# Kernel tuning notes

Measured on AMD Instinct MI355X. Metric: run time of the kernel, lower is better.

The kernel has to match this reference:

```python
import jax, jax.numpy as jnp
import numpy as np

B, S, D = 2, 2048, 1024
H, DQK, DV = 16, 64, 64
DECAY = 0.85


def _fractal_weights(seq_len: int, decay: float) -> np.ndarray:
    # Dragon-curve hierarchical weights: earlier (coarser) positions get higher
    # weight; weight decays by `decay` per hierarchy level. Normalized to sum 1,
    # matching DragonCurveGenerator.get_hierarchical_weights semantics.
    idx = np.arange(seq_len)
    level = np.floor(np.log2(idx + 1)).astype(np.int32)
    w = decay ** level.astype(np.float32)
    return (w / w.sum()).astype(np.float32)


def setup_inputs() -> dict:
    key = jax.random.key(0)
    kx, kq, kk, kv, ko = jax.random.split(key, 5)
    s = 1.0 / np.sqrt(D)
    return {
        "x": jax.random.normal(kx, (B, S, D), dtype=jnp.float32),
        "Wq": jax.random.normal(kq, (D, H * DQK), dtype=jnp.float32) * s,
        "Wk": jax.random.normal(kk, (D, H * DQK), dtype=jnp.float32) * s,
        "Wv": jax.random.normal(kv, (D, H * DV), dtype=jnp.float32) * s,
        "Wo": jax.random.normal(ko, (H * DV, D), dtype=jnp.float32) * s,
        "fractal_weights": jnp.asarray(_fractal_weights(S, DECAY)),
    }


def reference(x, Wq, Wk, Wv, Wo, fractal_weights):
    b, s, _ = x.shape
    # Projections (Linear with bias=False); weights stored as (in, out).
    Q = (x @ Wq).reshape(b, s, H, DQK).transpose(0, 2, 1, 3)  # [B,H,S,Dqk]
    K = (x @ Wk).reshape(b, s, H, DQK).transpose(0, 2, 1, 3)
    V = (x @ Wv).reshape(b, s, H, DV).transpose(0, 2, 1, 3)   # [B,H,S,Dv]
    scale = 1.0 / jnp.sqrt(jnp.asarray(DQK, dtype=x.dtype))
    scores = jnp.einsum("bhqd,bhkd->bhqk", Q, K) * scale      # [B,H,S,S]
    # Multiplicative per-key fractal bias applied BEFORE softmax.
    scores = scores * fractal_weights[None, None, None, :]
    attn = jax.nn.softmax(scores, axis=-1)
    out = jnp.einsum("bhqk,bhkd->bhqd", attn, V)               # [B,H,S,Dv]
    out = out.transpose(0, 2, 1, 3).reshape(b, s, H * DV)
    return out @ Wo                                            # [B,S,D]
```

## Files before the change

kernel.cpp:

```cpp
#include <hip/hip_runtime.h>
#include <hip/hip_bf16.h>
#include <stdint.h>

#define B_  2
#define S_  2048
#define D_  1024
#define H_  16
#define DH_ 64

typedef __attribute__((ext_vector_type(8))) __bf16    bf16x8;
typedef __attribute__((ext_vector_type(8))) _Float16  f16x8;
typedef __attribute__((ext_vector_type(4))) _Float16  f16x4;
typedef __attribute__((ext_vector_type(2))) __fp16    fp16x2;
typedef __attribute__((ext_vector_type(4))) float     f32x4;

__device__ inline unsigned short f2bf(float f) {
    union { float f; uint32_t u; } v; v.f = f;
    uint32_t r = (v.u + 0x7fffu + ((v.u >> 16) & 1u)) >> 16;
    return (unsigned short)r;
}

__device__ __forceinline__ void g2l16(const unsigned short* g, unsigned short* l) {
    __builtin_amdgcn_global_load_lds(
        (const __attribute__((address_space(1))) unsigned int*)g,
        (__attribute__((address_space(3))) unsigned int*)l,
        16, 0, 0);
}


__global__ void convert_x(const float* __restrict__ x, unsigned short* __restrict__ xb, int n) {
    int i = (blockIdx.x * blockDim.x + threadIdx.x) * 4;
    if (i < n) {
        float4 v = *(const float4*)(x + i);
        ushort4 o;
        o.x = f2bf(v.x); o.y = f2bf(v.y); o.z = f2bf(v.z); o.w = f2bf(v.w);
        *(ushort4*)(xb + i) = o;
    }
}

__global__ void transpose_w(const float* __restrict__ s0, const float* __restrict__ s1,
                            const float* __restrict__ s2, const float* __restrict__ s3,
                            unsigned short* __restrict__ d0, unsigned short* __restrict__ d1,
                            unsigned short* __restrict__ d2, unsigned short* __restrict__ d3) {
    __shared__ float tile[32][33];
    const float* src; unsigned short* dst;
    switch (blockIdx.z) {
        case 0: src = s0; dst = d0; break;
        case 1: src = s1; dst = d1; break;
        case 2: src = s2; dst = d2; break;
        default: src = s3; dst = d3; break;
    }
    int n0 = blockIdx.x * 32, k0 = blockIdx.y * 32;
    int tx = threadIdx.x, ty = threadIdx.y;
    for (int j = 0; j < 32; j += 8)
        tile[ty + j][tx] = src[(long)(k0 + ty + j) * 1024 + n0 + tx];
    __syncthreads();
    for (int j = 0; j < 32; j += 8)
        dst[(long)(n0 + ty + j) * 1024 + k0 + tx] = f2bf(tile[tx][ty + j]);
}

template<int MODE>
__global__ __launch_bounds__(256, 2)
void gemm128(const unsigned short* __restrict__ A, const unsigned short* __restrict__ Bt,
             unsigned short* __restrict__ Qo, unsigned short* __restrict__ Ko,
             unsigned short* __restrict__ Vt, float* __restrict__ Cout,
             const float* __restrict__ fw)
{
    __shared__ __align__(16) unsigned short As[128 * 64];
    __shared__ __align__(16) unsigned short Bs[128 * 64];
    const int tid  = threadIdx.x;
    const int lane = tid & 63, wid = tid >> 6;
    const int quad = lane >> 4, l15 = lane & 15;
    const int wm = wid >> 1, wn = wid & 1;
    const int bm = blockIdx.y, bn = blockIdx.x;
    const int K = 1024;
    f32x4 acc[4][4] = {};
    const long Abase = (long)bm * 128 * K;
    const long Bbase = (long)bn * 128 * K;

    for (int k0 = 0; k0 < K; k0 += 64) {
        __syncthreads();
#pragma unroll
        for (int i = 0; i < 4; i++) {
            int slot = i * 256 + wid * 64 + lane;
            int row = slot >> 3, cp = slot & 7;
            int c = cp ^ (row & 7);
            g2l16(A + Abase + (long)row * K + k0 + c * 8, &As[(i * 256 + wid * 64) * 8]);
        }
#pragma unroll
        for (int i = 0; i < 4; i++) {
            int slot = i * 256 + wid * 64 + lane;
            int row = slot >> 3, cp = slot & 7;
            int c = cp ^ (row & 7);
            g2l16(Bt + Bbase + (long)row * K + k0 + c * 8, &Bs[(i * 256 + wid * 64) * 8]);
        }
        __syncthreads();
#pragma unroll
        for (int ks = 0; ks < 2; ks++) {
            bf16x8 af[4], bfr[4];
#pragma unroll
            for (int t = 0; t < 4; t++) {
                int ra = wm * 64 + t * 16 + l15;
                af[t]  = *(const bf16x8*)(As + ra * 64 + (((ks * 4 + quad) ^ (l15 & 7))) * 8);
                int rb = wn * 64 + t * 16 + l15;
                bfr[t] = *(const bf16x8*)(Bs + rb * 64 + (((ks * 4 + quad) ^ (l15 & 7))) * 8);
            }
#pragma unroll
            for (int tm = 0; tm < 4; tm++)
#pragma unroll
                for (int tn = 0; tn < 4; tn++)
                    acc[tm][tn] = __builtin_amdgcn_mfma_f32_16x16x32_bf16(af[tm], bfr[tn], acc[tm][tn], 0, 0, 0);
        }
    }

    const float Cq = 0.125f * 1.44269504f;
    for (int tm = 0; tm < 4; tm++)
        for (int tn = 0; tn < 4; tn++)
            for (int r = 0; r < 4; r++) {
                int gm = bm * 128 + wm * 64 + tm * 16 + quad * 4 + r;
                int gn = bn * 128 + wn * 64 + tn * 16 + l15;
                float v = acc[tm][tn][r];
                if (MODE == 0) {
                    int b = gm >> 11, s = gm & 2047;
                    if (gn < 1024) {
                        int h = gn >> 6, d = gn & 63;
                        Qo[(((long)(b * H_ + h) * S_ + s) << 6) + d] = f2bf(v * Cq);
                    } else if (gn < 2048) {
                        int g = gn - 1024; int h = g >> 6, d = g & 63;
                        Ko[(((long)(b * H_ + h) * S_ + s) << 6) + d] = f2bf(v * fw[s]);
                    } else {
                        int g = gn - 2048; int h = g >> 6, d = g & 63;
                        union { _Float16 h; unsigned short u; } cv;
                        cv.h = (_Float16)v;
                        Vt[((long)(b * H_ + h) * DH_ + d) * S_ + s] = cv.u;
                    }
                } else {
                    Cout[(long)gm * 1024 + gn] = v;
                }
            }
}

__global__ __launch_bounds__(256, 4)
void attn_kernel(const unsigned short* __restrict__ Q, const unsigned short* __restrict__ Kb,
                 const unsigned short* __restrict__ Vt,
                 unsigned short* __restrict__ O)
{
    __shared__ __align__(16) unsigned short Ks[2][64 * 64];
    __shared__ __align__(16) unsigned short Vs[2][64 * 64];

    const int tid  = threadIdx.x;
    const int lane = tid & 63, wid = tid >> 6;
    const int quad = lane >> 4, l15 = lane & 15;
    const int bh = blockIdx.y;
    const int qt = blockIdx.x;

    const unsigned short* Kg = Kb + (long)bh * S_ * DH_;
    const unsigned short* Vg = Vt + (long)bh * (long)DH_ * S_;

    bf16x8 qf[2][2];
#pragma unroll
    for (int s = 0; s < 2; s++) {
        const unsigned short* Qp = Q + ((long)bh * S_ + qt * 128 + wid * 32 + s * 16 + l15) * DH_ + quad * 8;
        qf[s][0] = *(const bf16x8*)(Qp);
        qf[s][1] = *(const bf16x8*)(Qp + 32);
    }

    auto issue = [&](int buf, int kt) {
#pragma unroll
        for (int i = 0; i < 2; i++) {
            int base = i * 256 + wid * 64;
            int slot = base + lane;
            int row = slot >> 3, cp = slot & 7;
            int c = cp ^ (row & 7);
            g2l16(Kg + ((long)(kt * 64 + row) * 64 + c * 8), &Ks[buf][base * 8]);
        }
#pragma unroll
        for (int i = 0; i < 2; i++) {
            int base = i * 256 + wid * 64;
            int slot = base + lane;
            int row = slot >> 3, cp = slot & 7;
            int c = cp ^ (row & 7);
            g2l16(Vg + ((long)row * S_ + kt * 64 + c * 8), &Vs[buf][base * 8]);
        }
    };

    f32x4 oacc[2][4] = {};
    float l_r[2] = {0.f, 0.f};

    issue(0, 0);
    __syncthreads();

    for (int kt = 0; kt < S_ / 64; kt++) {
        const int cur = kt & 1;
        if (kt + 1 < S_ / 64) issue(1 - cur, kt + 1);

        const unsigned short* Kc = &Ks[cur][0];
        const unsigned short* Vc = &Vs[cur][0];

        f32x4 sacc[2][4] = {};
#pragma unroll
        for (int kc = 0; kc < 4; kc++) {
            int row = kc * 16 + l15;
            bf16x8 k0 = *(const bf16x8*)(Kc + (row * 8 + (quad       ^ (l15 & 7))) * 8);
            bf16x8 k1 = *(const bf16x8*)(Kc + (row * 8 + ((4 + quad) ^ (l15 & 7))) * 8);
#pragma unroll
            for (int s = 0; s < 2; s++) {
                sacc[s][kc] = __builtin_amdgcn_mfma_f32_16x16x32_bf16(k0, qf[s][0], sacc[s][kc], 0, 0, 0);
                sacc[s][kc] = __builtin_amdgcn_mfma_f32_16x16x32_bf16(k1, qf[s][1], sacc[s][kc], 0, 0, 0);
            }
        }

        f16x8 pk8[2][2];
#pragma unroll
        for (int s = 0; s < 2; s++)
#pragma unroll
            for (int c = 0; c < 2; c++) {
                union { uint4 u; f16x8 v; } pku;
#pragma unroll
                for (int h = 0; h < 2; h++) {
                    float p0 = __builtin_amdgcn_exp2f(sacc[s][2 * c + h][0]);
                    float p1 = __builtin_amdgcn_exp2f(sacc[s][2 * c + h][1]);
                    float p2 = __builtin_amdgcn_exp2f(sacc[s][2 * c + h][2]);
                    float p3 = __builtin_amdgcn_exp2f(sacc[s][2 * c + h][3]);
                    l_r[s] += (p0 + p1) + (p2 + p3);
                    union { fp16x2 h2; unsigned int u; } a, b;
                    a.h2 = __builtin_amdgcn_cvt_pkrtz(p0, p1);
                    b.h2 = __builtin_amdgcn_cvt_pkrtz(p2, p3);
                    if (h == 0) { pku.u.x = a.u; pku.u.y = b.u; }
                    else        { pku.u.z = a.u; pku.u.w = b.u; }
                }
                pk8[s][c] = pku.v;
            }

#pragma unroll
        for (int c = 0; c < 2; c++)
#pragma unroll
            for (int dt = 0; dt < 4; dt++) {
                int row = dt * 16 + l15;
                int p0 = (c * 4 +     (quad >> 1)) ^ (l15 & 7);
                int p1 = (c * 4 + 2 + (quad >> 1)) ^ (l15 & 7);
                f16x4 v0 = *(const f16x4*)(Vc + row * 64 + p0 * 8 + (quad & 1) * 4);
                f16x4 v1 = *(const f16x4*)(Vc + row * 64 + p1 * 8 + (quad & 1) * 4);
                f16x8 vf8 = __builtin_shufflevector(v0, v1, 0, 1, 2, 3, 4, 5, 6, 7);
                oacc[0][dt] = __builtin_amdgcn_mfma_f32_16x16x32_f16(pk8[0][c], vf8, oacc[0][dt], 0, 0, 0);
                oacc[1][dt] = __builtin_amdgcn_mfma_f32_16x16x32_f16(pk8[1][c], vf8, oacc[1][dt], 0, 0, 0);
            }

        __syncthreads();
    }

#pragma unroll
    for (int s = 0; s < 2; s++) {
        l_r[s] += __shfl_xor(l_r[s], 16);
        l_r[s] += __shfl_xor(l_r[s], 32);
    }

    int b = bh >> 4, h = bh & 15;
#pragma unroll
    for (int s = 0; s < 2; s++)
#pragma unroll
        for (int r = 0; r < 4; r++) {
            float inv = 1.0f / __shfl(l_r[s], quad * 4 + r);
            int srow = qt * 128 + wid * 32 + s * 16 + quad * 4 + r;
#pragma unroll
            for (int dt = 0; dt < 4; dt++)
                O[((long)(b * S_ + srow)) * 1024 + h * DH_ + dt * 16 + l15] = f2bf(oacc[s][dt][r] * inv);
        }
}


extern "C" void kernel_launch(void* const* d_in, const int* in_sizes, int n_in,
                              void* d_out, int out_size, void* d_ws, size_t ws_size,
                              hipStream_t stream)
{
    const float* x  = (const float*)d_in[0];
    const float* Wq = (const float*)d_in[1];
    const float* Wk = (const float*)d_in[2];
    const float* Wv = (const float*)d_in[3];
    const float* Wo = (const float*)d_in[4];
    const float* fw = (const float*)d_in[5];
    float* out = (float*)d_out;

    char* ws = (char*)d_ws;
    unsigned short* xb    = (unsigned short*)(ws);
    unsigned short* WqkvT = (unsigned short*)(ws + 8388608);
    unsigned short* WoT   = (unsigned short*)(ws + 14680064);
    unsigned short* Qb    = (unsigned short*)(ws + 16777216);
    unsigned short* Kb    = (unsigned short*)(ws + 25165824);
    unsigned short* Vt    = (unsigned short*)(ws + 33554432);
    unsigned short* Ob    = xb;

    convert_x<<<dim3((B_ * S_ * D_) / 4 / 256), dim3(256), 0, stream>>>(x, xb, B_ * S_ * D_);
    transpose_w<<<dim3(32, 32, 4), dim3(32, 8), 0, stream>>>(
        Wq, Wk, Wv, Wo,
        WqkvT, WqkvT + 1024 * 1024, WqkvT + 2 * 1024 * 1024, WoT);
    gemm128<0><<<dim3(24, 32), dim3(256), 0, stream>>>(xb, WqkvT, Qb, Kb, Vt, (float*)nullptr, fw);
    attn_kernel<<<dim3(S_ / 128, B_ * H_), dim3(256), 0, stream>>>(Qb, Kb, Vt, Ob);
    gemm128<1><<<dim3(8, 32), dim3(256), 0, stream>>>(Ob, WoT,
        (unsigned short*)nullptr, (unsigned short*)nullptr, (unsigned short*)nullptr, out, (const float*)nullptr);
}
```

Before: 203.3 us.

## Halve attention query tile per block and swizzle V layout against LDS bank conflicts

The attention kernel now gives each block 64 query rows instead of 128, with one 16-row sub-tile per wave. This doubles the grid to 1024 blocks for better occupancy and CU coverage, and halves accumulator registers. The cost is twice the K/V tile loads from global memory per query. Separately, the QKV GEMM epilogue stores V^T with an XOR swizzle of the sequence index on bit 2 keyed by d&8, and the attention V reads apply a matching half-offset, meant to avoid LDS bank conflicts on f16x4 reads.

```diff
diff --git a/kernel.cpp b/kernel.cpp
--- a/kernel.cpp
+++ b/kernel.cpp
@@ -132,7 +132,8 @@
                         int g = gn - 2048; int h = g >> 6, d = g & 63;
                         union { _Float16 h; unsigned short u; } cv;
                         cv.h = (_Float16)v;
-                        Vt[((long)(b * H_ + h) * DH_ + d) * S_ + s] = cv.u;
+                        int sp = s ^ ((d & 8) ? 4 : 0);
+                        Vt[((long)(b * H_ + h) * DH_ + d) * S_ + sp] = cv.u;
                     }
                 } else {
                     Cout[(long)gm * 1024 + gn] = v;
@@ -157,12 +158,11 @@
     const unsigned short* Kg = Kb + (long)bh * S_ * DH_;
     const unsigned short* Vg = Vt + (long)bh * (long)DH_ * S_;
 
-    bf16x8 qf[2][2];
-#pragma unroll
-    for (int s = 0; s < 2; s++) {
-        const unsigned short* Qp = Q + ((long)bh * S_ + qt * 128 + wid * 32 + s * 16 + l15) * DH_ + quad * 8;
-        qf[s][0] = *(const bf16x8*)(Qp);
-        qf[s][1] = *(const bf16x8*)(Qp + 32);
+    bf16x8 qf[2];
+    {
+        const unsigned short* Qp = Q + ((long)bh * S_ + qt * 64 + wid * 16 + l15) * DH_ + quad * 8;
+        qf[0] = *(const bf16x8*)(Qp);
+        qf[1] = *(const bf16x8*)(Qp + 32);
     }
 
     auto issue = [&](int buf, int kt) {
@@ -184,8 +184,8 @@
         }
     };
 
-    f32x4 oacc[2][4] = {};
-    float l_r[2] = {0.f, 0.f};
+    f32x4 oacc[4] = {};
+    float l_r = 0.f;
 
     issue(0, 0);
     __syncthreads();
@@ -197,41 +197,37 @@
         const unsigned short* Kc = &Ks[cur][0];
         const unsigned short* Vc = &Vs[cur][0];
 
-        f32x4 sacc[2][4] = {};
+        f32x4 sacc[4] = {};
 #pragma unroll
         for (int kc = 0; kc < 4; kc++) {
             int row = kc * 16 + l15;
             bf16x8 k0 = *(const bf16x8*)(Kc + (row * 8 + (quad       ^ (l15 & 7))) * 8);
             bf16x8 k1 = *(const bf16x8*)(Kc + (row * 8 + ((4 + quad) ^ (l15 & 7))) * 8);
-#pragma unroll
-            for (int s = 0; s < 2; s++) {
-                sacc[s][kc] = __builtin_amdgcn_mfma_f32_16x16x32_bf16(k0, qf[s][0], sacc[s][kc], 0, 0, 0);
-                sacc[s][kc] = __builtin_amdgcn_mfma_f32_16x16x32_bf16(k1, qf[s][1], sacc[s][kc], 0, 0, 0);
-            }
-        }
-
-        f16x8 pk8[2][2];
-#pragma unroll
-        for (int s = 0; s < 2; s++)
-#pragma unroll
-            for (int c = 0; c < 2; c++) {
-                union { uint4 u; f16x8 v; } pku;
-#pragma unroll
-                for (int h = 0; h < 2; h++) {
-                    float p0 = __builtin_amdgcn_exp2f(sacc[s][2 * c + h][0]);
-                    float p1 = __builtin_amdgcn_exp2f(sacc[s][2 * c + h][1]);
-                    float p2 = __builtin_amdgcn_exp2f(sacc[s][2 * c + h][2]);
-                    float p3 = __builtin_amdgcn_exp2f(sacc[s][2 * c + h][3]);
-                    l_r[s] += (p0 + p1) + (p2 + p3);
-                    union { fp16x2 h2; unsigned int u; } a, b;
-                    a.h2 = __builtin_amdgcn_cvt_pkrtz(p0, p1);
-                    b.h2 = __builtin_amdgcn_cvt_pkrtz(p2, p3);
-                    if (h == 0) { pku.u.x = a.u; pku.u.y = b.u; }
-                    else        { pku.u.z = a.u; pku.u.w = b.u; }
-                }
-                pk8[s][c] = pku.v;
-            }
-
+            sacc[kc] = __builtin_amdgcn_mfma_f32_16x16x32_bf16(k0, qf[0], sacc[kc], 0, 0, 0);
+            sacc[kc] = __builtin_amdgcn_mfma_f32_16x16x32_bf16(k1, qf[1], sacc[kc], 0, 0, 0);
+        }
+
+        f16x8 pk8[2];
+#pragma unroll
+        for (int c = 0; c < 2; c++) {
+            union { uint4 u; f16x8 v; } pku;
+#pragma unroll
+            for (int h = 0; h < 2; h++) {
+                float p0 = __builtin_amdgcn_exp2f(sacc[2 * c + h][0]);
+                float p1 = __builtin_amdgcn_exp2f(sacc[2 * c + h][1]);
+                float p2 = __builtin_amdgcn_exp2f(sacc[2 * c + h][2]);
+                float p3 = __builtin_amdgcn_exp2f(sacc[2 * c + h][3]);
+                l_r += (p0 + p1) + (p2 + p3);
+                union { fp16x2 h2; unsigned int u; } a, b;
+                a.h2 = __builtin_amdgcn_cvt_pkrtz(p0, p1);
+                b.h2 = __builtin_amdgcn_cvt_pkrtz(p2, p3);
+                if (h == 0) { pku.u.x = a.u; pku.u.y = b.u; }
+                else        { pku.u.z = a.u; pku.u.w = b.u; }
+            }
+            pk8[c] = pku.v;
+        }
+
+        const int hf = (((quad & 1) ^ ((l15 >> 3) & 1))) * 4;
 #pragma unroll
         for (int c = 0; c < 2; c++)
 #pragma unroll
@@ -239,33 +235,27 @@
                 int row = dt * 16 + l15;
                 int p0 = (c * 4 +     (quad >> 1)) ^ (l15 & 7);
                 int p1 = (c * 4 + 2 + (quad >> 1)) ^ (l15 & 7);
-                f16x4 v0 = *(const f16x4*)(Vc + row * 64 + p0 * 8 + (quad & 1) * 4);
-                f16x4 v1 = *(const f16x4*)(Vc + row * 64 + p1 * 8 + (quad & 1) * 4);
+                f16x4 v0 = *(const f16x4*)(Vc + row * 64 + p0 * 8 + hf);
+                f16x4 v1 = *(const f16x4*)(Vc + row * 64 + p1 * 8 + hf);
                 f16x8 vf8 = __builtin_shufflevector(v0, v1, 0, 1, 2, 3, 4, 5, 6, 7);
-                oacc[0][dt] = __builtin_amdgcn_mfma_f32_16x16x32_f16(pk8[0][c], vf8, oacc[0][dt], 0, 0, 0);
-                oacc[1][dt] = __builtin_amdgcn_mfma_f32_16x16x32_f16(pk8[1][c], vf8, oacc[1][dt], 0, 0, 0);
+                oacc[dt] = __builtin_amdgcn_mfma_f32_16x16x32_f16(pk8[c], vf8, oacc[dt], 0, 0, 0);
             }
 
         __syncthreads();
     }
 
-#pragma unroll
-    for (int s = 0; s < 2; s++) {
-        l_r[s] += __shfl_xor(l_r[s], 16);
-        l_r[s] += __shfl_xor(l_r[s], 32);
-    }
+    l_r += __shfl_xor(l_r, 16);
+    l_r += __shfl_xor(l_r, 32);
 
     int b = bh >> 4, h = bh & 15;
 #pragma unroll
-    for (int s = 0; s < 2; s++)
-#pragma unroll
-        for (int r = 0; r < 4; r++) {
-            float inv = 1.0f / __shfl(l_r[s], quad * 4 + r);
-            int srow = qt * 128 + wid * 32 + s * 16 + quad * 4 + r;
-#pragma unroll
-            for (int dt = 0; dt < 4; dt++)
-                O[((long)(b * S_ + srow)) * 1024 + h * DH_ + dt * 16 + l15] = f2bf(oacc[s][dt][r] * inv);
-        }
+    for (int r = 0; r < 4; r++) {
+        float inv = 1.0f / __shfl(l_r, quad * 4 + r);
+        int srow = qt * 64 + wid * 16 + quad * 4 + r;
+#pragma unroll
+        for (int dt = 0; dt < 4; dt++)
+            O[((long)(b * S_ + srow)) * 1024 + h * DH_ + dt * 16 + l15] = f2bf(oacc[dt][r] * inv);
+    }
 }
 
 
@@ -295,7 +285,7 @@
         Wq, Wk, Wv, Wo,
         WqkvT, WqkvT + 1024 * 1024, WqkvT + 2 * 1024 * 1024, WoT);
     gemm128<0><<<dim3(24, 32), dim3(256), 0, stream>>>(xb, WqkvT, Qb, Kb, Vt, (float*)nullptr, fw);
-    attn_kernel<<<dim3(S_ / 128, B_ * H_), dim3(256), 0, stream>>>(Qb, Kb, Vt, Ob);
+    attn_kernel<<<dim3(S_ / 64, B_ * H_), dim3(256), 0, stream>>>(Qb, Kb, Vt, Ob);
     gemm128<1><<<dim3(8, 32), dim3(256), 0, stream>>>(Ob, WoT,
         (unsigned short*)nullptr, (unsigned short*)nullptr, (unsigned short*)nullptr, out, (const float*)nullptr);
 }
```

After: 193.4 us. 1.05x faster.

## Split attention key range across two wave groups and merge partials in shared memory

Applied to the files above, without the earlier changes.

The attention block grows to 512 threads. Two halves of four waves each process 16 key tiles apiece for the same 128 queries, and half 1 writes its partial outputs and row sums to LDS for half 0 to combine. Row sums now come from an MFMA against a vector of ones instead of scalar adds. The V layout written by the QKV GEMM gets a column XOR swizzle that the new LDS read offsets match, to reduce bank conflicts. This doubles the waves per tile and shortens the serial key loop, at the cost of twice the LDS per block and an extra reduction step.

```diff
diff --git a/kernel.cpp b/kernel.cpp
--- a/kernel.cpp
+++ b/kernel.cpp
@@ -132,7 +132,8 @@
                         int g = gn - 2048; int h = g >> 6, d = g & 63;
                         union { _Float16 h; unsigned short u; } cv;
                         cv.h = (_Float16)v;
-                        Vt[((long)(b * H_ + h) * DH_ + d) * S_ + s] = cv.u;
+                        int sp = s ^ ((d & 8) ? 4 : 0);
+                        Vt[((long)(b * H_ + h) * DH_ + d) * S_ + sp] = cv.u;
                     }
                 } else {
                     Cout[(long)gm * 1024 + gn] = v;
@@ -140,16 +141,16 @@
             }
 }
 
-__global__ __launch_bounds__(256, 4)
+__global__ __launch_bounds__(512, 4)
 void attn_kernel(const unsigned short* __restrict__ Q, const unsigned short* __restrict__ Kb,
                  const unsigned short* __restrict__ Vt,
                  unsigned short* __restrict__ O)
 {
-    __shared__ __align__(16) unsigned short Ks[2][64 * 64];
-    __shared__ __align__(16) unsigned short Vs[2][64 * 64];
+    __shared__ __align__(16) unsigned short smem[2][2][2][64 * 64];
 
     const int tid  = threadIdx.x;
     const int lane = tid & 63, wid = tid >> 6;
+    const int half = wid >> 2, sw = wid & 3;
     const int quad = lane >> 4, l15 = lane & 15;
     const int bh = blockIdx.y;
     const int qt = blockIdx.x;
@@ -159,43 +160,46 @@
 
     bf16x8 qf[2][2];
 #pragma unroll
-    for (int s = 0; s < 2; s++) {
-        const unsigned short* Qp = Q + ((long)bh * S_ + qt * 128 + wid * 32 + s * 16 + l15) * DH_ + quad * 8;
-        qf[s][0] = *(const bf16x8*)(Qp);
-        qf[s][1] = *(const bf16x8*)(Qp + 32);
+    for (int st = 0; st < 2; st++) {
+        const unsigned short* Qp = Q + ((long)bh * S_ + qt * 128 + sw * 32 + st * 16 + l15) * DH_ + quad * 8;
+        qf[st][0] = *(const bf16x8*)(Qp);
+        qf[st][1] = *(const bf16x8*)(Qp + 32);
     }
 
     auto issue = [&](int buf, int kt) {
 #pragma unroll
         for (int i = 0; i < 2; i++) {
-            int base = i * 256 + wid * 64;
+            int base = i * 256 + sw * 64;
             int slot = base + lane;
             int row = slot >> 3, cp = slot & 7;
             int c = cp ^ (row & 7);
-            g2l16(Kg + ((long)(kt * 64 + row) * 64 + c * 8), &Ks[buf][base * 8]);
+            g2l16(Kg + ((long)(kt * 64 + row) * 64 + c * 8), &smem[half][buf][0][base * 8]);
         }
 #pragma unroll
         for (int i = 0; i < 2; i++) {
-            int base = i * 256 + wid * 64;
+            int base = i * 256 + sw * 64;
             int slot = base + lane;
             int row = slot >> 3, cp = slot & 7;
             int c = cp ^ (row & 7);
-            g2l16(Vg + ((long)row * S_ + kt * 64 + c * 8), &Vs[buf][base * 8]);
+            g2l16(Vg + ((long)row * S_ + kt * 64 + c * 8), &smem[half][buf][1][base * 8]);
         }
     };
 
     f32x4 oacc[2][4] = {};
-    float l_r[2] = {0.f, 0.f};
-
-    issue(0, 0);
+    f32x4 lacc[2] = {};
+    const f16x8 vone = {(_Float16)1.f, (_Float16)1.f, (_Float16)1.f, (_Float16)1.f,
+                        (_Float16)1.f, (_Float16)1.f, (_Float16)1.f, (_Float16)1.f};
+
+    const int kt0 = half * 16;
+    issue(0, kt0);
     __syncthreads();
 
-    for (int kt = 0; kt < S_ / 64; kt++) {
-        const int cur = kt & 1;
-        if (kt + 1 < S_ / 64) issue(1 - cur, kt + 1);
-
-        const unsigned short* Kc = &Ks[cur][0];
-        const unsigned short* Vc = &Vs[cur][0];
+    for (int t = 0; t < 16; t++) {
+        const int cur = t & 1;
+        if (t + 1 < 16) issue(1 - cur, kt0 + t + 1);
+
+        const unsigned short* Kc = &smem[half][cur][0][0];
+        const unsigned short* Vc = &smem[half][cur][1][0];
 
         f32x4 sacc[2][4] = {};
 #pragma unroll
@@ -204,68 +208,92 @@
             bf16x8 k0 = *(const bf16x8*)(Kc + (row * 8 + (quad       ^ (l15 & 7))) * 8);
             bf16x8 k1 = *(const bf16x8*)(Kc + (row * 8 + ((4 + quad) ^ (l15 & 7))) * 8);
 #pragma unroll
-            for (int s = 0; s < 2; s++) {
-                sacc[s][kc] = __builtin_amdgcn_mfma_f32_16x16x32_bf16(k0, qf[s][0], sacc[s][kc], 0, 0, 0);
-                sacc[s][kc] = __builtin_amdgcn_mfma_f32_16x16x32_bf16(k1, qf[s][1], sacc[s][kc], 0, 0, 0);
+            for (int st = 0; st < 2; st++) {
+                sacc[st][kc] = __builtin_amdgcn_mfma_f32_16x16x32_bf16(k0, qf[st][0], sacc[st][kc], 0, 0, 0);
+                sacc[st][kc] = __builtin_amdgcn_mfma_f32_16x16x32_bf16(k1, qf[st][1], sacc[st][kc], 0, 0, 0);
             }
         }
 
         f16x8 pk8[2][2];
 #pragma unroll
-        for (int s = 0; s < 2; s++)
+        for (int st = 0; st < 2; st++)
 #pragma unroll
             for (int c = 0; c < 2; c++) {
                 union { uint4 u; f16x8 v; } pku;
 #pragma unroll
-                for (int h = 0; h < 2; h++) {
-                    float p0 = __builtin_amdgcn_exp2f(sacc[s][2 * c + h][0]);
-                    float p1 = __builtin_amdgcn_exp2f(sacc[s][2 * c + h][1]);
-                    float p2 = __builtin_amdgcn_exp2f(sacc[s][2 * c + h][2]);
-                    float p3 = __builtin_amdgcn_exp2f(sacc[s][2 * c + h][3]);
-                    l_r[s] += (p0 + p1) + (p2 + p3);
+                for (int hh = 0; hh < 2; hh++) {
+                    float p0 = __builtin_amdgcn_exp2f(sacc[st][2 * c + hh][0]);
+                    float p1 = __builtin_amdgcn_exp2f(sacc[st][2 * c + hh][1]);
+                    float p2 = __builtin_amdgcn_exp2f(sacc[st][2 * c + hh][2]);
+                    float p3 = __builtin_amdgcn_exp2f(sacc[st][2 * c + hh][3]);
                     union { fp16x2 h2; unsigned int u; } a, b;
                     a.h2 = __builtin_amdgcn_cvt_pkrtz(p0, p1);
                     b.h2 = __builtin_amdgcn_cvt_pkrtz(p2, p3);
-                    if (h == 0) { pku.u.x = a.u; pku.u.y = b.u; }
-                    else        { pku.u.z = a.u; pku.u.w = b.u; }
+                    if (hh == 0) { pku.u.x = a.u; pku.u.y = b.u; }
+                    else         { pku.u.z = a.u; pku.u.w = b.u; }
                 }
-                pk8[s][c] = pku.v;
-            }
-
-#pragma unroll
-        for (int c = 0; c < 2; c++)
+                pk8[st][c] = pku.v;
+            }
+
+        const int hf = (((quad & 1) ^ ((l15 >> 3) & 1))) * 4;
+#pragma unroll
+        for (int c = 0; c < 2; c++) {
+            lacc[0] = __builtin_amdgcn_mfma_f32_16x16x32_f16(pk8[0][c], vone, lacc[0], 0, 0, 0);
+            lacc[1] = __builtin_amdgcn_mfma_f32_16x16x32_f16(pk8[1][c], vone, lacc[1], 0, 0, 0);
 #pragma unroll
             for (int dt = 0; dt < 4; dt++) {
                 int row = dt * 16 + l15;
                 int p0 = (c * 4 +     (quad >> 1)) ^ (l15 & 7);
                 int p1 = (c * 4 + 2 + (quad >> 1)) ^ (l15 & 7);
-                f16x4 v0 = *(const f16x4*)(Vc + row * 64 + p0 * 8 + (quad & 1) * 4);
-                f16x4 v1 = *(const f16x4*)(Vc + row * 64 + p1 * 8 + (quad & 1) * 4);
+                f16x4 v0 = *(const f16x4*)(Vc + row * 64 + p0 * 8 + hf);
+                f16x4 v1 = *(const f16x4*)(Vc + row * 64 + p1 * 8 + hf);
                 f16x8 vf8 = __builtin_shufflevector(v0, v1, 0, 1, 2, 3, 4, 5, 6, 7);
                 oacc[0][dt] = __builtin_amdgcn_mfma_f32_16x16x32_f16(pk8[0][c], vf8, oacc[0][dt], 0, 0, 0);
                 oacc[1][dt] = __builtin_amdgcn_mfma_f32_16x16x32_f16(pk8[1][c], vf8, oacc[1][dt], 0, 0, 0);
             }
+        }
 
         __syncthreads();
     }
 
-#pragma unroll
-    for (int s = 0; s < 2; s++) {
-        l_r[s] += __shfl_xor(l_r[s], 16);
-        l_r[s] += __shfl_xor(l_r[s], 32);
-    }
-
-    int b = bh >> 4, h = bh & 15;
-#pragma unroll
-    for (int s = 0; s < 2; s++)
-#pragma unroll
-        for (int r = 0; r < 4; r++) {
-            float inv = 1.0f / __shfl(l_r[s], quad * 4 + r);
-            int srow = qt * 128 + wid * 32 + s * 16 + quad * 4 + r;
+    float* ov = (float*)&smem[0][0][0][0];
+    float* lv = ov + 128 * 66;
+
+    if (half == 1) {
+#pragma unroll
+        for (int st = 0; st < 2; st++) {
 #pragma unroll
             for (int dt = 0; dt < 4; dt++)
-                O[((long)(b * S_ + srow)) * 1024 + h * DH_ + dt * 16 + l15] = f2bf(oacc[s][dt][r] * inv);
-        }
+#pragma unroll
+                for (int r = 0; r < 4; r++) {
+                    int qr = sw * 32 + st * 16 + quad * 4 + r;
+                    ov[qr * 66 + dt * 16 + l15] = oacc[st][dt][r];
+                }
+            if (l15 == 0) {
+#pragma unroll
+                for (int r = 0; r < 4; r++)
+                    lv[sw * 32 + st * 16 + quad * 4 + r] = lacc[st][r];
+            }
+        }
+    }
+    __syncthreads();
+
+    if (half == 0) {
+        int b = bh >> 4, h = bh & 15;
+#pragma unroll
+        for (int st = 0; st < 2; st++)
+#pragma unroll
+            for (int r = 0; r < 4; r++) {
+                int qr = sw * 32 + st * 16 + quad * 4 + r;
+                float inv = 1.0f / (lacc[st][r] + lv[qr]);
+                int srow = qt * 128 + qr;
+#pragma unroll
+                for (int dt = 0; dt < 4; dt++) {
+                    float val = oacc[st][dt][r] + ov[qr * 66 + dt * 16 + l15];
+                    O[((long)(b * S_ + srow)) * 1024 + h * DH_ + dt * 16 + l15] = f2bf(val * inv);
+                }
+            }
+    }
 }
 
 
@@ -295,7 +323,7 @@
         Wq, Wk, Wv, Wo,
         WqkvT, WqkvT + 1024 * 1024, WqkvT + 2 * 1024 * 1024, WoT);
     gemm128<0><<<dim3(24, 32), dim3(256), 0, stream>>>(xb, WqkvT, Qb, Kb, Vt, (float*)nullptr, fw);
-    attn_kernel<<<dim3(S_ / 128, B_ * H_), dim3(256), 0, stream>>>(Qb, Kb, Vt, Ob);
+    attn_kernel<<<dim3(S_ / 128, B_ * H_), dim3(512), 0, stream>>>(Qb, Kb, Vt, Ob);
     gemm128<1><<<dim3(8, 32), dim3(256), 0, stream>>>(Ob, WoT,
         (unsigned short*)nullptr, (unsigned short*)nullptr, (unsigned short*)nullptr, out, (const float*)nullptr);
 }
```

Result: faster. 185.9 us (-8.6%).
